# Performance work log

Hardware: AMD Instinct MI355X
Metric: run time of the kernel (lower is better)

## Reference

```python
import jax, jax.numpy as jnp
import numpy as np

B, S, H = 1, 4096, 2048
NH, HD = 16, 128  # num_heads, head_dim = H // NH


def setup_inputs() -> dict:
    key = jax.random.key(0)
    k1, k2, k3 = jax.random.split(key, 3)
    x = jax.random.normal(k1, (B, S, H), dtype=jnp.float32)
    w_qkv = jax.random.normal(k2, (3 * H, H), dtype=jnp.float32) * (1.0 / np.sqrt(H))
    w_out = jax.random.normal(k3, (H, H), dtype=jnp.float32) * (1.0 / np.sqrt(H))
    return {"x": x, "w_qkv": w_qkv, "w_out": w_out}


def reference(x, w_qkv, w_out):
    b, s, _ = x.shape
    # qkv projection: torch Linear computes x @ W^T
    qkv = jnp.einsum('bsh,oh->bso', x, w_qkv)
    qkv = qkv.reshape(b, s, 3, NH, HD).transpose(2, 0, 3, 1, 4)  # [3,B,NH,S,HD]
    q, k, v = qkv[0], qkv[1], qkv[2]
    # world_size == 1 -> single ring step == full attention with online softmax
    scores = jnp.einsum('bhqd,bhkd->bhqk', q, k) / np.sqrt(HD)
    m = jnp.max(scores, axis=-1, keepdims=True)          # running max (single step)
    p = jnp.exp(scores - m)                              # scores_exp
    out = jnp.einsum('bhqk,bhkd->bhqd', p, v)
    denom = jnp.sum(p, axis=-1, keepdims=True) + 1e-8    # running_sum + eps
    out = out / denom
    out = out.transpose(0, 2, 1, 3).reshape(b, s, H)     # [B,S,H]
    return jnp.einsum('bsh,oh->bso', out, w_out)
```

## Files before the change

### kernel.cpp

```cpp
#include <hip/hip_runtime.h>
#include <stdint.h>

typedef __attribute__((ext_vector_type(4))) float f32x4;
typedef __attribute__((ext_vector_type(16))) float f32x16;
typedef __attribute__((ext_vector_type(8))) short bf16x8;
typedef unsigned short u16;

#define MFMA(a, b, c) __builtin_amdgcn_mfma_f32_16x16x32_bf16(a, b, c, 0, 0, 0)
#define MFMA32(a, b, c) __builtin_amdgcn_mfma_f32_32x32x16_bf16(a, b, c, 0, 0, 0)
#define EXP2(x) __builtin_amdgcn_exp2f(x)
#define FENCE asm volatile("" ::: "memory")
#define BARRIER do { FENCE; __builtin_amdgcn_s_barrier(); FENCE; } while (0)

__device__ __forceinline__ u16 f2bf(float f) {
  union { float f; unsigned u; } x; x.f = f;
  unsigned r = x.u + 0x7fffu + ((x.u >> 16) & 1u);
  return (u16)(r >> 16);
}

__device__ __forceinline__ unsigned cvtpk(float lo, float hi) {
  unsigned r;
  asm("v_cvt_pk_bf16_f32 %0, %1, %2" : "=v"(r) : "v"(lo), "v"(hi));
  return r;
}

__device__ __forceinline__ void pl32swap(unsigned& a, unsigned& b) {
  asm volatile("v_permlane32_swap_b32 %0, %1" : "+v"(a), "+v"(b));
}

__device__ __forceinline__ void gload16(const void* g, void* l) {
  __builtin_amdgcn_global_load_lds(
      (const __attribute__((address_space(1))) unsigned int*)g,
      (__attribute__((address_space(3))) unsigned int*)l, 16, 0, 0);
}

__global__ void __launch_bounds__(256) cast_bf16(const float* __restrict__ in,
                                                 u16* __restrict__ out, int n4) {
  int i = blockIdx.x * 256 + threadIdx.x;
  if (i >= n4) return;
  float4 v = reinterpret_cast<const float4*>(in)[i];
  ushort4 o;
  o.x = f2bf(v.x); o.y = f2bf(v.y); o.z = f2bf(v.z); o.w = f2bf(v.w);
  reinterpret_cast<ushort4*>(out)[i] = o;
}

template <int EPI>
__global__ void __launch_bounds__(512)
gemm8(const u16* __restrict__ A, const u16* __restrict__ B,
      void* __restrict__ C0, void* __restrict__ C1, void* __restrict__ C2,
      int M, int N, int K, int MBt) {
  __shared__ alignas(16) char smb[131072];
  const int tid = threadIdx.x;
  const int w = tid >> 6, lane = tid & 63;
  const int lr = lane & 15, g = lane >> 4;
  const int wm = w >> 2, wn = w & 3;
  const int gb = (blockIdx.x & 7) * ((int)gridDim.x >> 3) + (blockIdx.x >> 3);
  const int mb = gb % MBt, nb = gb / MBt;
  const int m0 = mb * 256, n0 = nb * 256;
  const int NT = K >> 6, NIT = NT >> 1;

  const int l8 = lane >> 3, l7 = lane & 7;
  const int csb = (l7 ^ l8) * 16;
  const char* asrcb[2];
  const char* bsrcb[2];
  unsigned adst[2], bdst[2];
#pragma unroll
  for (int j = 0; j < 2; ++j) {
    int c = 2 * w + j;
    int ra = (c & 7) * 8 + ((c >> 3) << 7) + l8;
    asrcb[j] = (const char*)(A + (size_t)(m0 + ra) * K) + csb;
    adst[j] = (unsigned)(ra * 128 + l7 * 16);
    int rb = (c & 3) * 8 + ((c >> 2) << 6) + l8;
    bsrcb[j] = (const char*)(B + (size_t)(n0 + rb) * K) + csb;
    bdst[j] = (unsigned)(rb * 128 + l7 * 16);
  }
  const size_t arow64 = (size_t)64 * K * 2;
  const size_t brow32 = (size_t)32 * K * 2;

#define STG(kt, u)                                                            \
  do {                                                                        \
    if ((kt) < NT) {                                                          \
      int _d = ((kt) & 1) ? 32768 : 0;                                        \
      size_t _ko = (size_t)(kt) * 128;                                        \
      if ((u) == 0) {                                                         \
        gload16(asrcb[0] + _ko, smb + _d + adst[0]);                          \
        gload16(asrcb[1] + _ko, smb + _d + adst[1]);                          \
      } else if ((u) == 1) {                                                  \
        gload16(bsrcb[0] + _ko, smb + 65536 + _d + bdst[0]);                  \
        gload16(bsrcb[1] + _ko, smb + 65536 + _d + bdst[1]);                  \
      } else if ((u) == 2) {                                                  \
        gload16(asrcb[0] + arow64 + _ko, smb + _d + 8192 + adst[0]);          \
        gload16(asrcb[1] + arow64 + _ko, smb + _d + 8192 + adst[1]);          \
      } else {                                                                \
        gload16(bsrcb[0] + brow32 + _ko, smb + 65536 + _d + 4096 + bdst[0]);  \
        gload16(bsrcb[1] + brow32 + _ko, smb + 65536 + _d + 4096 + bdst[1]);  \
      }                                                                       \
    }                                                                         \
  } while (0)

  f32x4 acc[8][4];
#pragma unroll
  for (int x = 0; x < 8; ++x)
#pragma unroll
    for (int y = 0; y < 4; ++y) acc[x][y] = f32x4{0.f, 0.f, 0.f, 0.f};
  bf16x8 af[4][2], bf01[2][2], bf23[2][2];
  const int aoff0 = ((g) ^ (lr & 7)) << 4;
  const int aoff1 = ((4 + g) ^ (lr & 7)) << 4;
  const int arow = (wm * 128 + lr) * 128;
  const int brow = (wn * 64 + lr) * 128;

  auto LDA = [&](const char* base, int mih) {
#pragma unroll
    for (int mi = 0; mi < 4; ++mi) {
      const char* p = base + arow + (mih * 64 + mi * 16) * 128;
      af[mi][0] = *(const bf16x8*)(p + aoff0);
      af[mi][1] = *(const bf16x8*)(p + aoff1);
    }
  };
  auto LDB = [&](const char* base, bf16x8 (*bfr)[2], int nih) {
#pragma unroll
    for (int ni = 0; ni < 2; ++ni) {
      const char* p = base + brow + (nih * 32 + ni * 16) * 128;
      bfr[ni][0] = *(const bf16x8*)(p + aoff0);
      bfr[ni][1] = *(const bf16x8*)(p + aoff1);
    }
  };
  auto MM = [&](int mih, int nih, bf16x8 (*bfr)[2]) {
    __builtin_amdgcn_s_setprio(1);
#pragma unroll
    for (int mi = 0; mi < 4; ++mi)
#pragma unroll
      for (int ni = 0; ni < 2; ++ni) {
        acc[mih * 4 + mi][nih * 2 + ni] =
            MFMA(af[mi][0], bfr[ni][0], acc[mih * 4 + mi][nih * 2 + ni]);
        acc[mih * 4 + mi][nih * 2 + ni] =
            MFMA(af[mi][1], bfr[ni][1], acc[mih * 4 + mi][nih * 2 + ni]);
      }
    __builtin_amdgcn_s_setprio(0);
  };

  STG(0, 0); STG(0, 1); STG(0, 2); STG(0, 3);
  STG(1, 0); STG(1, 1); STG(1, 2);
  asm volatile("s_waitcnt vmcnt(6)" ::: "memory");
  BARRIER;

  const char* A0 = smb;
  const char* B0 = smb + 65536;
  const char* A1 = smb + 32768;
  const char* B1 = smb + 65536 + 32768;

  for (int it = 0; it < NIT; ++it) {
    const int t0 = 2 * it;
    const bool lastit = (it == NIT - 1);
    LDA(A0, 0); LDB(B0, bf01, 0); STG(t0 + 1, 3);
    BARRIER; MM(0, 0, bf01); BARRIER;
    LDB(B0, bf23, 1); STG(t0 + 2, 0);
    BARRIER; MM(0, 1, bf23); BARRIER;
    LDA(A0, 1); STG(t0 + 2, 1);
    BARRIER; MM(1, 1, bf23); BARRIER;
    STG(t0 + 2, 2);
    if (lastit) asm volatile("s_waitcnt vmcnt(0)" ::: "memory");
    else        asm volatile("s_waitcnt vmcnt(6)" ::: "memory");
    BARRIER; MM(1, 0, bf01); BARRIER;
    LDA(A1, 0); LDB(B1, bf01, 0); STG(t0 + 2, 3);
    BARRIER; MM(0, 0, bf01); BARRIER;
    LDB(B1, bf23, 1); STG(t0 + 3, 0);
    BARRIER; MM(0, 1, bf23); BARRIER;
    LDA(A1, 1); STG(t0 + 3, 1);
    BARRIER; MM(1, 1, bf23); BARRIER;
    STG(t0 + 3, 2);
    asm volatile("s_waitcnt vmcnt(6)" ::: "memory");
    BARRIER; MM(1, 0, bf01); BARRIER;
  }
#undef STG

  if (EPI == 0) {
    const float qs = 0.08838834764831845f * 1.4426950408889634f;
    u16* qo = (u16*)C0;
    u16* ko = (u16*)C1;
    u16* vo = (u16*)C2;
#pragma unroll
    for (int mi = 0; mi < 8; ++mi) {
      int s0 = m0 + wm * 128 + mi * 16 + g * 4;
#pragma unroll
      for (int ni = 0; ni < 4; ++ni) {
        int n = n0 + wn * 64 + ni * 16 + lr;
        int t = n >> 11, hh = (n >> 7) & 15, d = n & 127;
        if (t == 2) {
          ushort4 pk;
          pk.x = f2bf(acc[mi][ni][0]);
          pk.y = f2bf(acc[mi][ni][1]);
          pk.z = f2bf(acc[mi][ni][2]);
          pk.w = f2bf(acc[mi][ni][3]);
          *(ushort4*)(vo + (size_t)(hh * 128 + d) * 4096 + s0) = pk;
        } else {
          float sc = (t == 0) ? qs : 1.f;
          u16* dq = (t == 0 ? qo : ko) + (size_t)(hh * 4096 + s0) * 128 + d;
#pragma unroll
          for (int j = 0; j < 4; ++j) dq[(size_t)j * 128] = f2bf(acc[mi][ni][j] * sc);
        }
      }
    }
  } else {
    float* C = (float*)C0;
#pragma unroll
    for (int mi = 0; mi < 8; ++mi)
#pragma unroll
      for (int ni = 0; ni < 4; ++ni) {
        size_t r0 = (size_t)(m0 + wm * 128 + mi * 16 + g * 4);
        int cn = n0 + wn * 64 + ni * 16 + lr;
#pragma unroll
        for (int j = 0; j < 4; ++j) C[(r0 + j) * N + cn] = acc[mi][ni][j];
      }
  }
}

__global__ void __launch_bounds__(512)
attn_kernel(const u16* __restrict__ qg, const u16* __restrict__ kg,
            const u16* __restrict__ vtg, u16* __restrict__ og) {
  __shared__ alignas(64) char smb[131072];
  const int tid = threadIdx.x;
  const int w = tid >> 6, lane = tid & 63;
  const int ql = lane & 31, hl = lane >> 5;
  const int gb = (blockIdx.x & 7) * 32 + (blockIdx.x >> 3);
  const int h = gb >> 4;
  const int qb = gb & 15;

  const u16* ssrc[8];
  unsigned sdst[8];
  size_t sstep;
  if (w < 4) {
    sstep = 128 * 128;
#pragma unroll
    for (int i = 0; i < 8; ++i) {
      int c = w * 8 + i;
      int r = c * 4 + (lane >> 4);
      int sb = (lane & 15) ^ (r & 15);
      ssrc[i] = kg + (size_t)(h * 4096 + r) * 128 + sb * 8;
      sdst[i] = c * 1024;
    }
  } else {
    sstep = 128;
#pragma unroll
    for (int i = 0; i < 8; ++i) {
      int c = (w - 4) * 8 + i;
      int r = c * 4 + (lane >> 4);
      int sb = (lane & 15) ^ (r & 15);
      ssrc[i] = vtg + (size_t)(h * 128 + r) * 4096 + sb * 8;
      sdst[i] = 65536 + c * 1024;
    }
  }

  const u16* qrow = qg + (size_t)(h * 4096 + qb * 256 + w * 32 + ql) * 128 + hl * 8;
  bf16x8 qf[8];
#pragma unroll
  for (int s = 0; s < 8; ++s) qf[s] = *(const bf16x8*)(qrow + s * 16);

  f32x16 of[4];
#pragma unroll
  for (int i = 0; i < 4; ++i)
#pragma unroll
    for (int r = 0; r < 16; ++r) of[i][r] = 0.f;
  float mrun = -1e30f, lsum = 0.f;
  const float thr = 6.0f;

#pragma unroll
  for (int i = 0; i < 8; ++i) gload16(ssrc[i], smb + sdst[i]);

  const int kxor = (ql & 15) << 4;
  for (int t = 0; t < 32; ++t) {
    const int cur = t & 1;
    asm volatile("s_waitcnt vmcnt(0)" ::: "memory");
    __builtin_amdgcn_s_barrier();
    FENCE;
    if (t + 1 < 32) {
      const int nb = (t + 1) & 1;
#pragma unroll
      for (int i = 0; i < 8; ++i)
        gload16(ssrc[i] + (size_t)(t + 1) * sstep, smb + sdst[i] + nb * 32768);
    }
    const char* kbuf = smb + cur * 32768;
    const char* vbuf = smb + 65536 + cur * 32768;

    f32x16 st[4];
#pragma unroll
    for (int kb = 0; kb < 4; ++kb)
#pragma unroll
      for (int r = 0; r < 16; ++r) st[kb][r] = 0.f;
    __builtin_amdgcn_s_setprio(1);
#pragma unroll
    for (int s = 0; s < 8; ++s) {
      int off = ((s * 2 + hl) << 4) ^ kxor;
      bf16x8 k0 = *(const bf16x8*)(kbuf + (0 * 32 + ql) * 256 + off);
      bf16x8 k1 = *(const bf16x8*)(kbuf + (1 * 32 + ql) * 256 + off);
      bf16x8 k2 = *(const bf16x8*)(kbuf + (2 * 32 + ql) * 256 + off);
      bf16x8 k3 = *(const bf16x8*)(kbuf + (3 * 32 + ql) * 256 + off);
      st[0] = MFMA32(k0, qf[s], st[0]);
      st[1] = MFMA32(k1, qf[s], st[1]);
      st[2] = MFMA32(k2, qf[s], st[2]);
      st[3] = MFMA32(k3, qf[s], st[3]);
    }
    __builtin_amdgcn_s_setprio(0);

    float tmax = -1e30f;
#pragma unroll
    for (int kb = 0; kb < 4; ++kb)
#pragma unroll
      for (int r = 0; r < 16; ++r) tmax = fmaxf(tmax, st[kb][r]);
    tmax = fmaxf(tmax, __shfl_xor(tmax, 32));
    if (!__all(tmax - mrun <= thr)) {
      float mnew = fmaxf(mrun, tmax);
      float esc = EXP2(mrun - mnew);
#pragma unroll
      for (int db = 0; db < 4; ++db)
#pragma unroll
        for (int r = 0; r < 16; ++r) of[db][r] *= esc;
      lsum *= esc;
      mrun = mnew;
    }
    float psum = 0.f;
    union U { unsigned u[4]; bf16x8 v; };
    U paf[8];
#pragma unroll
    for (int gp = 0; gp < 2; ++gp) {
      unsigned pk0[8], pk1[8];
#pragma unroll
      for (int i = 0; i < 8; ++i) {
        float a0 = EXP2(st[2 * gp + 0][2 * i] - mrun);
        float b0 = EXP2(st[2 * gp + 0][2 * i + 1] - mrun);
        float a1 = EXP2(st[2 * gp + 1][2 * i] - mrun);
        float b1 = EXP2(st[2 * gp + 1][2 * i + 1] - mrun);
        psum += (a0 + b0) + (a1 + b1);
        pk0[i] = cvtpk(a0, b0);
        pk1[i] = cvtpk(a1, b1);
      }
      pl32swap(pk0[0], pk0[2]); pl32swap(pk0[1], pk0[3]);
      pl32swap(pk0[4], pk0[6]); pl32swap(pk0[5], pk0[7]);
      pl32swap(pk1[0], pk1[2]); pl32swap(pk1[1], pk1[3]);
      pl32swap(pk1[4], pk1[6]); pl32swap(pk1[5], pk1[7]);
#pragma unroll
      for (int i = 0; i < 4; ++i) {
        paf[gp * 4 + 0].u[i] = pk0[i];
        paf[gp * 4 + 1].u[i] = pk0[4 + i];
        paf[gp * 4 + 2].u[i] = pk1[i];
        paf[gp * 4 + 3].u[i] = pk1[4 + i];
      }
    }
    psum += __shfl_xor(psum, 32);
    lsum += psum;

    __builtin_amdgcn_s_setprio(1);
#pragma unroll
    for (int db = 0; db < 4; ++db) {
      const char* vrow = vbuf + (db * 32 + ql) * 256;
#pragma unroll
      for (int kp = 0; kp < 8; ++kp) {
        int m = (kp * 2 + hl) ^ (ql & 15);
        bf16x8 vf = *(const bf16x8*)(vrow + m * 16);
        of[db] = MFMA32(vf, paf[kp].v, of[db]);
      }
    }
    __builtin_amdgcn_s_setprio(0);
    FENCE;
  }

  float linv = 1.f / (lsum + 1e-8f);
  size_t qrow_o = (size_t)(qb * 256 + w * 32 + ql) * 2048 + h * 128;
#pragma unroll
  for (int db = 0; db < 4; ++db)
#pragma unroll
    for (int u = 0; u < 4; ++u) {
      ushort4 pk;
      pk.x = f2bf(of[db][4 * u + 0] * linv);
      pk.y = f2bf(of[db][4 * u + 1] * linv);
      pk.z = f2bf(of[db][4 * u + 2] * linv);
      pk.w = f2bf(of[db][4 * u + 3] * linv);
      *(ushort4*)(og + qrow_o + db * 32 + 8 * u + hl * 4) = pk;
    }
}

extern "C" void kernel_launch(void* const* d_in, const int* in_sizes, int n_in,
                              void* d_out, int out_size, void* d_ws, size_t ws_size,
                              hipStream_t stream) {
  const float* x = (const float*)d_in[0];
  const float* w_qkv = (const float*)d_in[1];
  const float* w_out = (const float*)d_in[2];

  char* ws = (char*)d_ws;
  u16* xb = (u16*)(ws + 0);
  u16* wqkvb = (u16*)(ws + 16777216);
  u16* woutb = (u16*)(ws + 41943040);
  u16* qb = (u16*)(ws + 50331648);
  u16* kb = (u16*)(ws + 67108864);
  u16* vtb = (u16*)(ws + 83886080);
  u16* aob = (u16*)(ws + 100663296);

  cast_bf16<<<8192, 256, 0, stream>>>(x, xb, 2097152);
  cast_bf16<<<12288, 256, 0, stream>>>(w_qkv, wqkvb, 3145728);
  cast_bf16<<<4096, 256, 0, stream>>>(w_out, woutb, 1048576);

  gemm8<0><<<384, 512, 0, stream>>>(xb, wqkvb, qb, kb, vtb, 4096, 6144, 2048, 16);
  attn_kernel<<<256, 512, 0, stream>>>(qb, kb, vtb, aob);
  gemm8<1><<<128, 512, 0, stream>>>(aob, woutb, d_out, nullptr, nullptr, 4096, 2048, 2048, 16);
}
```

Before: 339.1 us.

## Software-pipeline attention QK/PV across tiles and use smaller-tile output GEMM

The attention loop is restructured so the QK^T product for tile u+1 is interleaved with the PV product for tile u. K is prefetched two tiles ahead and V one tile ahead, and the output rescale is deferred to the next iteration. This aims to hide softmax latency behind MFMA work. Separately, the output projection switches from the 256x256-tile gemm8 with 128 blocks to a new 128x128-tile gemm_bt kernel with 512 blocks and a simple single-buffered loop. That gives more parallelism but less data reuse and no load/compute overlap.

```diff
diff --git a/kernel.cpp b/kernel.cpp
--- a/kernel.cpp
+++ b/kernel.cpp
@@ -215,6 +215,76 @@
   }
 }
 
+template <int EPI>
+__global__ void __launch_bounds__(256, 2)
+gemm_bt(const u16* __restrict__ A, const u16* __restrict__ B,
+        void* __restrict__ C0, void* __restrict__ C1, void* __restrict__ C2,
+        int M, int N, int K, int MB) {
+  __shared__ alignas(16) u16 sm[8192];
+  const int tid = threadIdx.x;
+  const int w = tid >> 6, lane = tid & 63;
+  const int lr = lane & 15, g = lane >> 4;
+  const int gb = (blockIdx.x & 7) * ((int)gridDim.x >> 3) + (blockIdx.x >> 3);
+  const int mb = gb % MB, nb = gb / MB;
+  const int m0 = mb * 128, n0 = nb * 128;
+
+  const u16* src[4];
+  u16* dst[4];
+#pragma unroll
+  for (int i = 0; i < 4; ++i) {
+    int c = w * 4 + i;
+    int r = (c & 7) * 16 + (lane >> 2);
+    int sb = (lane & 3) ^ ((r >> 1) & 3);
+    src[i] = (c < 8) ? (A + (size_t)(m0 + r) * K + sb * 8)
+                     : (B + (size_t)(n0 + r) * K + sb * 8);
+    dst[i] = &sm[c * 512];
+  }
+
+  f32x4 acc[4][4];
+#pragma unroll
+  for (int x = 0; x < 4; ++x)
+#pragma unroll
+    for (int y = 0; y < 4; ++y) acc[x][y] = f32x4{0.f, 0.f, 0.f, 0.f};
+
+  const int rowb = (w >> 1) * 64, colb = (w & 1) * 64;
+  const int nk = K >> 5;
+  for (int kt = 0; kt < nk; ++kt) {
+#pragma unroll
+    for (int i = 0; i < 4; ++i) gload16(src[i] + kt * 32, dst[i]);
+    __syncthreads();
+    bf16x8 af[4], bfr[4];
+#pragma unroll
+    for (int mi = 0; mi < 4; ++mi) {
+      int r = rowb + mi * 16 + lr;
+      af[mi] = *(const bf16x8*)((const char*)sm + r * 64 +
+                                ((g * 16) ^ (((r >> 1) & 3) << 4)));
+    }
+#pragma unroll
+    for (int ni = 0; ni < 4; ++ni) {
+      int r = colb + ni * 16 + lr;
+      bfr[ni] = *(const bf16x8*)((const char*)sm + 8192 + r * 64 +
+                                 ((g * 16) ^ (((r >> 1) & 3) << 4)));
+    }
+#pragma unroll
+    for (int mi = 0; mi < 4; ++mi)
+#pragma unroll
+      for (int ni = 0; ni < 4; ++ni)
+        acc[mi][ni] = MFMA(af[mi], bfr[ni], acc[mi][ni]);
+    __syncthreads();
+  }
+
+  float* C = (float*)C0;
+#pragma unroll
+  for (int mi = 0; mi < 4; ++mi)
+#pragma unroll
+    for (int ni = 0; ni < 4; ++ni) {
+      size_t r0 = (size_t)(m0 + rowb + mi * 16 + g * 4);
+      int cn = n0 + colb + ni * 16 + lr;
+#pragma unroll
+      for (int j = 0; j < 4; ++j) C[(r0 + j) * N + cn] = acc[mi][ni][j];
+    }
+}
+
 __global__ void __launch_bounds__(512)
 attn_kernel(const u16* __restrict__ qg, const u16* __restrict__ kg,
             const u16* __restrict__ vtg, u16* __restrict__ og) {
@@ -263,45 +333,15 @@
     for (int r = 0; r < 16; ++r) of[i][r] = 0.f;
   float mrun = -1e30f, lsum = 0.f;
   const float thr = 6.0f;
-
-#pragma unroll
-  for (int i = 0; i < 8; ++i) gload16(ssrc[i], smb + sdst[i]);
-
   const int kxor = (ql & 15) << 4;
-  for (int t = 0; t < 32; ++t) {
-    const int cur = t & 1;
-    asm volatile("s_waitcnt vmcnt(0)" ::: "memory");
-    __builtin_amdgcn_s_barrier();
-    FENCE;
-    if (t + 1 < 32) {
-      const int nb = (t + 1) & 1;
-#pragma unroll
-      for (int i = 0; i < 8; ++i)
-        gload16(ssrc[i] + (size_t)(t + 1) * sstep, smb + sdst[i] + nb * 32768);
-    }
-    const char* kbuf = smb + cur * 32768;
-    const char* vbuf = smb + 65536 + cur * 32768;
-
-    f32x16 st[4];
-#pragma unroll
-    for (int kb = 0; kb < 4; ++kb)
-#pragma unroll
-      for (int r = 0; r < 16; ++r) st[kb][r] = 0.f;
-    __builtin_amdgcn_s_setprio(1);
-#pragma unroll
-    for (int s = 0; s < 8; ++s) {
-      int off = ((s * 2 + hl) << 4) ^ kxor;
-      bf16x8 k0 = *(const bf16x8*)(kbuf + (0 * 32 + ql) * 256 + off);
-      bf16x8 k1 = *(const bf16x8*)(kbuf + (1 * 32 + ql) * 256 + off);
-      bf16x8 k2 = *(const bf16x8*)(kbuf + (2 * 32 + ql) * 256 + off);
-      bf16x8 k3 = *(const bf16x8*)(kbuf + (3 * 32 + ql) * 256 + off);
-      st[0] = MFMA32(k0, qf[s], st[0]);
-      st[1] = MFMA32(k1, qf[s], st[1]);
-      st[2] = MFMA32(k2, qf[s], st[2]);
-      st[3] = MFMA32(k3, qf[s], st[3]);
-    }
-    __builtin_amdgcn_s_setprio(0);
-
+
+  union U { unsigned u[4]; bf16x8 v; };
+  U paf[8];
+  float escc = 1.f;
+  bool rflag = false;
+
+  f32x16 st[4];
+  auto SM = [&]() {
     float tmax = -1e30f;
 #pragma unroll
     for (int kb = 0; kb < 4; ++kb)
@@ -310,17 +350,14 @@
     tmax = fmaxf(tmax, __shfl_xor(tmax, 32));
     if (!__all(tmax - mrun <= thr)) {
       float mnew = fmaxf(mrun, tmax);
-      float esc = EXP2(mrun - mnew);
-#pragma unroll
-      for (int db = 0; db < 4; ++db)
-#pragma unroll
-        for (int r = 0; r < 16; ++r) of[db][r] *= esc;
-      lsum *= esc;
+      escc = EXP2(mrun - mnew);
+      lsum *= escc;
       mrun = mnew;
+      rflag = true;
+    } else {
+      rflag = false;
     }
     float psum = 0.f;
-    union U { unsigned u[4]; bf16x8 v; };
-    U paf[8];
 #pragma unroll
     for (int gp = 0; gp < 2; ++gp) {
       unsigned pk0[8], pk1[8];
@@ -348,19 +385,98 @@
     }
     psum += __shfl_xor(psum, 32);
     lsum += psum;
-
-    __builtin_amdgcn_s_setprio(1);
-#pragma unroll
-    for (int db = 0; db < 4; ++db) {
-      const char* vrow = vbuf + (db * 32 + ql) * 256;
-#pragma unroll
-      for (int kp = 0; kp < 8; ++kp) {
-        int m = (kp * 2 + hl) ^ (ql & 15);
-        bf16x8 vf = *(const bf16x8*)(vrow + m * 16);
-        of[db] = MFMA32(vf, paf[kp].v, of[db]);
-      }
-    }
-    __builtin_amdgcn_s_setprio(0);
+  };
+
+  auto QKs = [&](const char* kbuf, int s) {
+    int off = ((s * 2 + hl) << 4) ^ kxor;
+    bf16x8 k0 = *(const bf16x8*)(kbuf + (0 * 32 + ql) * 256 + off);
+    bf16x8 k1 = *(const bf16x8*)(kbuf + (1 * 32 + ql) * 256 + off);
+    bf16x8 k2 = *(const bf16x8*)(kbuf + (2 * 32 + ql) * 256 + off);
+    bf16x8 k3 = *(const bf16x8*)(kbuf + (3 * 32 + ql) * 256 + off);
+    st[0] = MFMA32(k0, qf[s], st[0]);
+    st[1] = MFMA32(k1, qf[s], st[1]);
+    st[2] = MFMA32(k2, qf[s], st[2]);
+    st[3] = MFMA32(k3, qf[s], st[3]);
+  };
+  auto PVdb = [&](const char* vbuf, int db) {
+    const char* vrow = vbuf + (db * 32 + ql) * 256;
+#pragma unroll
+    for (int kp = 0; kp < 8; ++kp) {
+      int m = (kp * 2 + hl) ^ (ql & 15);
+      bf16x8 vf = *(const bf16x8*)(vrow + m * 16);
+      of[db] = MFMA32(vf, paf[kp].v, of[db]);
+    }
+  };
+
+#pragma unroll
+  for (int i = 0; i < 8; ++i) gload16(ssrc[i], smb + sdst[i]);
+  asm volatile("s_waitcnt vmcnt(0)" ::: "memory");
+  BARRIER;
+  if (w < 4) {
+#pragma unroll
+    for (int i = 0; i < 8; ++i)
+      gload16(ssrc[i] + sstep, smb + sdst[i] + 32768);
+  }
+#pragma unroll
+  for (int kb = 0; kb < 4; ++kb)
+#pragma unroll
+    for (int r = 0; r < 16; ++r) st[kb][r] = 0.f;
+  __builtin_amdgcn_s_setprio(1);
+#pragma unroll
+  for (int s = 0; s < 8; ++s) QKs(smb, s);
+  __builtin_amdgcn_s_setprio(0);
+  SM();
+
+  for (int u = 0; u < 32; ++u) {
+    asm volatile("s_waitcnt vmcnt(0)" ::: "memory");
+    __builtin_amdgcn_s_barrier();
+    FENCE;
+    if (w < 4) {
+      if (u < 30) {
+        const int nb = u & 1;
+#pragma unroll
+        for (int i = 0; i < 8; ++i)
+          gload16(ssrc[i] + (size_t)(u + 2) * sstep, smb + sdst[i] + nb * 32768);
+      }
+    } else {
+      if (u < 31) {
+        const int nb = (u + 1) & 1;
+#pragma unroll
+        for (int i = 0; i < 8; ++i)
+          gload16(ssrc[i] + (size_t)(u + 1) * sstep, smb + sdst[i] + nb * 32768);
+      }
+    }
+    const char* kbuf = smb + ((u + 1) & 1) * 32768;
+    const char* vbuf = smb + 65536 + (u & 1) * 32768;
+
+    if (rflag) {
+#pragma unroll
+      for (int db = 0; db < 4; ++db)
+#pragma unroll
+        for (int r = 0; r < 16; ++r) of[db][r] *= escc;
+    }
+
+    if (u < 31) {
+#pragma unroll
+      for (int kb = 0; kb < 4; ++kb)
+#pragma unroll
+        for (int r = 0; r < 16; ++r) st[kb][r] = 0.f;
+      __builtin_amdgcn_s_setprio(1);
+#pragma unroll
+      for (int s = 0; s < 4; ++s) {
+        QKs(kbuf, s);
+        PVdb(vbuf, s);
+      }
+#pragma unroll
+      for (int s = 4; s < 8; ++s) QKs(kbuf, s);
+      __builtin_amdgcn_s_setprio(0);
+      SM();
+    } else {
+      __builtin_amdgcn_s_setprio(1);
+#pragma unroll
+      for (int db = 0; db < 4; ++db) PVdb(vbuf, db);
+      __builtin_amdgcn_s_setprio(0);
+    }
     FENCE;
   }
 
@@ -401,5 +517,5 @@
 
   gemm8<0><<<384, 512, 0, stream>>>(xb, wqkvb, qb, kb, vtb, 4096, 6144, 2048, 16);
   attn_kernel<<<256, 512, 0, stream>>>(qb, kb, vtb, aob);
-  gemm8<1><<<128, 512, 0, stream>>>(aob, woutb, d_out, nullptr, nullptr, 4096, 2048, 2048, 16);
-}
+  gemm_bt<1><<<512, 256, 0, stream>>>(aob, woutb, d_out, nullptr, nullptr, 4096, 2048, 2048, 32);
+}
```

After: 330.4 us. -2.6%, faster.
